# Kernel tuning notes

Measured on AMD Instinct MI355X. Metric: run time of the kernel, lower is better.

The kernel has to match this reference:

```python
import jax, jax.numpy as jnp
import numpy as np

H = 16        # num heads
DH = 128      # head dim
C = 64        # delta-rule chunk size
MAG = 0.5     # mag_weight
GATE_NORM = 16.0
EPS = 1e-6


def setup_inputs() -> dict:
    key = jax.random.key(0)
    ks = jax.random.split(key, 5)
    b, n, d = 2, 1024, H * DH
    s = d ** -0.5
    return {
        "x": jax.random.normal(ks[0], (b, n, d), jnp.float32),
        "Wq": jax.random.normal(ks[1], (d, d), jnp.float32) * s,
        "Wk": jax.random.normal(ks[2], (d, d), jnp.float32) * s,
        "Wv": jax.random.normal(ks[3], (d, d), jnp.float32) * s,
        "Wo": jax.random.normal(ks[4], (d, d), jnp.float32) * s,
    }


def _delta_rule_chunkwise(q, k, v, beta, chunk):
    # q,k,v: [b,h,l,d]; beta: [b,h,l,d] per-dim gate. Chunked DeltaNet parallel form.
    b, h, l, dk = q.shape
    dv = v.shape[-1]
    nc = l // chunk
    q = q * (dk ** -0.5)
    v = v * beta
    k_beta = k * beta
    qc, kc, vc, kbc = (a.reshape(b, h, nc, chunk, -1) for a in (q, k, v, k_beta))
    eye = jnp.eye(chunk, dtype=q.dtype)
    strict = jnp.tril(jnp.ones((chunk, chunk), bool), -1)
    # T = (I + strict_lower(k_beta k^T))^{-1} via triangular solve
    L = jnp.where(strict, kbc @ jnp.swapaxes(kc, -1, -2), 0.0)  # [b,h,nc,C,C]
    T = jax.scipy.linalg.solve_triangular(eye + L, jnp.broadcast_to(eye, L.shape), lower=True)
    u = T @ vc    # [b,h,nc,C,dv]
    w = T @ kbc   # [b,h,nc,C,dk]
    incl = jnp.tril(jnp.ones((chunk, chunk), bool))

    def step(S, inp):
        q_i, k_i, u_i, w_i = inp  # [b,h,C,d]
        u_i = u_i - w_i @ S
        attn = jnp.where(incl, q_i @ jnp.swapaxes(k_i, -1, -2), 0.0)
        o_i = q_i @ S + attn @ u_i
        S = S + jnp.swapaxes(k_i, -1, -2) @ u_i
        return S, o_i

    xs = tuple(jnp.moveaxis(a, 2, 0) for a in (qc, kc, u, w))
    S0 = jnp.zeros((b, h, dk, dv), q.dtype)
    S, o = jax.lax.scan(step, S0, xs)
    o = jnp.moveaxis(o, 0, 2).reshape(b, h, l, dv)
    return o, S


def _heads(t, b, n):
    return t.reshape(b, n, H, DH).transpose(0, 2, 1, 3)


def _base_attn(x, Wq, Wk, Wv, Wo):
    # vanilla causal softmax attention using the shared projections
    b, n, d = x.shape
    q, k, v = _heads(x @ Wq, b, n), _heads(x @ Wk, b, n), _heads(x @ Wv, b, n)
    scores = jnp.einsum('bhqd,bhkd->bhqk', q, k) / np.sqrt(DH).astype(np.float32)
    causal = jnp.tril(jnp.ones((n, n), bool))
    a = jax.nn.softmax(jnp.where(causal, scores, -jnp.inf), axis=-1)
    o = jnp.einsum('bhqk,bhkd->bhqd', a, v)
    return o.transpose(0, 2, 1, 3).reshape(b, n, d) @ Wo


def reference(x, Wq, Wk, Wv, Wo):
    b, n, d = x.shape
    k_raw = x @ Wk
    q = _heads(x @ Wq, b, n)
    k = _heads(k_raw, b, n)
    v = _heads(x @ Wv, b, n)
    g = _heads(k_raw, b, n)  # pool_g is identity: output_size == head_dim*num_kv_heads
    q = jnp.clip(jax.nn.softmax(q, axis=-1), EPS, 1.0 - EPS)
    k = jnp.clip(jax.nn.softmax(k, axis=-1), EPS, 1.0 - EPS)
    g = jnp.clip(jax.nn.log_sigmoid(g) / GATE_NORM, -GATE_NORM, GATE_NORM)
    o_lin, _ = _delta_rule_chunkwise(q.astype(jnp.float32), k.astype(jnp.float32),
                                     v.astype(jnp.float32), g.astype(jnp.float32), C)
    o_lin = o_lin.transpose(0, 2, 1, 3).reshape(b, n, d) @ Wo
    o_base = _base_attn(x, Wq, Wk, Wv, Wo)
    return MAG * o_lin + (1.0 - MAG) * o_base
```

## Files before the change

kernel.cpp:

```cpp
#include <hip/hip_runtime.h>
#include <hip/hip_bf16.h>
#include <math.h>

#define D 2048
#define NROWS 2048
#define NQKV 6144
#define H 16
#define DH 128
#define CHK 64
#define NC 16
#define EPSC 1e-6f
#define RSQDH 0.08838834764831845f

typedef unsigned short ushort_t;
typedef __attribute__((ext_vector_type(4))) float f4_t;
typedef __attribute__((ext_vector_type(8))) short s8_t;
typedef __attribute__((ext_vector_type(8))) _Float16 h8_t;
typedef __attribute__((ext_vector_type(4))) _Float16 h4_t;
typedef __attribute__((ext_vector_type(4))) unsigned short us4_t;

#define MFMA16(a, b, c) __builtin_amdgcn_mfma_f32_16x16x32_bf16((a), (b), (c), 0, 0, 0)
#define MFMAH(a, b, c)  __builtin_amdgcn_mfma_f32_16x16x32_f16((a), (b), (c), 0, 0, 0)
#define GLOAD16(g, l) __builtin_amdgcn_global_load_lds((const __attribute__((address_space(1))) unsigned int*)(g), (__attribute__((address_space(3))) unsigned int*)(l), 16, 0, 0)

__device__ __forceinline__ ushort_t f2bf(float f) {
  union { float f; unsigned u; } v; v.f = f;
  unsigned r = (v.u + 0x7fffu + ((v.u >> 16) & 1u)) >> 16;
  return (ushort_t)r;
}
__device__ __forceinline__ float bf2f(ushort_t h) {
  union { unsigned u; float f; } v; v.u = ((unsigned)h) << 16;
  return v.f;
}

__global__ __launch_bounds__(256) void split_h(const float* __restrict__ in,
                                               _Float16* __restrict__ hi) {
  int i = (blockIdx.x * 256 + threadIdx.x) * 4;
  float4 v = *(const float4*)(in + i);
  float vv[4] = {v.x, v.y, v.z, v.w};
  h4_t h;
#pragma unroll
  for (int j = 0; j < 4; j++) h[j] = (_Float16)vv[j];
  *(h4_t*)(hi + i) = h;
}

__global__ __launch_bounds__(256) void wsplit4(const float* __restrict__ Wq,
                                               const float* __restrict__ Wk,
                                               const float* __restrict__ Wv,
                                               const float* __restrict__ Wo,
                                               _Float16* __restrict__ Tqkv,
                                               _Float16* __restrict__ To) {
  __shared__ float t[32][33];
  const int tid = threadIdx.x;
  const int k0 = blockIdx.y * 32, n0 = blockIdx.x * 32;
  const int z = blockIdx.z;
  const float* W = (z == 0) ? Wq : (z == 1) ? Wk : (z == 2) ? Wv : Wo;
  _Float16* T = (z < 3) ? (Tqkv + (size_t)z * D * D) : To;
  const int c = tid & 31, rr = tid >> 5;
#pragma unroll
  for (int p = 0; p < 4; p++) {
    int r = p * 8 + rr;
    t[r][c] = W[(size_t)(k0 + r) * D + n0 + c];
  }
  __syncthreads();
#pragma unroll
  for (int p = 0; p < 4; p++) {
    int r = p * 8 + rr;
    T[(size_t)(n0 + r) * D + k0 + c] = (_Float16)t[c][r];
  }
}

__global__ __launch_bounds__(256) void gemm1(const _Float16* __restrict__ Ah,
                                             const _Float16* __restrict__ Bt,
                                             float* __restrict__ C,
                                             int M, int N, int K) {
  __shared__ __align__(16) ushort_t A_s[2][4096];
  __shared__ __align__(16) ushort_t B_s[2][4096];
  const int tid = threadIdx.x, lane = tid & 63, wid = tid >> 6;
  const int nwg = gridDim.x;
  int bid = blockIdx.x;
  int swz = (bid & 7) * (nwg >> 3) + (bid >> 3);
  const int nbn = N >> 7;
  const int bm = swz / nbn, bn = swz % nbn;
  const int row0 = bm << 7, col0 = bn << 7;
  const int lm = lane & 15, lg = lane >> 4;
  const int wrow = (wid >> 1) * 64, wcol = (wid & 1) * 64;
  const int NT = K >> 5;

  f4_t acc[4][4];
#pragma unroll
  for (int m = 0; m < 4; m++)
#pragma unroll
    for (int n = 0; n < 4; n++) acc[m][n] = (f4_t){0.f, 0.f, 0.f, 0.f};

  auto stage = [&](int buf, int ks) {
    int k0 = ks << 5;
#pragma unroll
    for (int p = 0; p < 2; p++) {
      int c = p * 256 + wid * 64 + lane;
      int r = c >> 2, q = (c & 3) * 8;
      char* la = (char*)&A_s[buf][0] + p * 4096 + wid * 1024;
      GLOAD16(Ah + (size_t)(row0 + r) * K + k0 + q, la);
      char* lb = (char*)&B_s[buf][0] + p * 4096 + wid * 1024;
      GLOAD16(Bt + (size_t)(col0 + r) * K + k0 + q, lb);
    }
  };

  stage(0, 0);
  __syncthreads();
  for (int t = 0; t < NT; t++) {
    int cur = t & 1;
    if (t + 1 < NT) stage(cur ^ 1, t + 1);
    h8_t af[4], bfr[4];
#pragma unroll
    for (int m = 0; m < 4; m++)
      af[m] = *(const h8_t*)&A_s[cur][(wrow + m * 16 + lm) * 32 + lg * 8];
#pragma unroll
    for (int n = 0; n < 4; n++)
      bfr[n] = *(const h8_t*)&B_s[cur][(wcol + n * 16 + lm) * 32 + lg * 8];
#pragma unroll
    for (int m = 0; m < 4; m++)
#pragma unroll
      for (int n = 0; n < 4; n++)
        acc[m][n] = MFMAH(af[m], bfr[n], acc[m][n]);
    __syncthreads();
  }
#pragma unroll
  for (int m = 0; m < 4; m++)
#pragma unroll
    for (int n = 0; n < 4; n++)
#pragma unroll
      for (int r = 0; r < 4; r++)
        C[(size_t)(row0 + wrow + m * 16 + lg * 4 + r) * N + col0 + wcol + n * 16 + lm] = acc[m][n][r];
}

__global__ __launch_bounds__(256) void gemm1h(const _Float16* __restrict__ Ah,
                                              const _Float16* __restrict__ Bt,
                                              _Float16* __restrict__ C,
                                              int M, int N, int K) {
  __shared__ __align__(16) ushort_t A_s[2][4096];
  __shared__ __align__(16) ushort_t B_s[2][4096];
  const int tid = threadIdx.x, lane = tid & 63, wid = tid >> 6;
  const int nwg = gridDim.x;
  int bid = blockIdx.x;
  int swz = (bid & 7) * (nwg >> 3) + (bid >> 3);
  const int nbn = N >> 7;
  const int bm = swz / nbn, bn = swz % nbn;
  const int lm = lane & 15, lg = lane >> 4;
  const int row0 = bm << 7, col0 = bn << 7;
  const int wrow = (wid >> 1) * 64, wcol = (wid & 1) * 64;
  const int NT = K >> 5;

  f4_t acc[4][4];
#pragma unroll
  for (int m = 0; m < 4; m++)
#pragma unroll
    for (int n = 0; n < 4; n++) acc[m][n] = (f4_t){0.f, 0.f, 0.f, 0.f};

  auto stage = [&](int buf, int ks) {
    int k0 = ks << 5;
#pragma unroll
    for (int p = 0; p < 2; p++) {
      int c = p * 256 + wid * 64 + lane;
      int r = c >> 2, q = (c & 3) * 8;
      char* la = (char*)&A_s[buf][0] + p * 4096 + wid * 1024;
      GLOAD16(Ah + (size_t)(row0 + r) * K + k0 + q, la);
      char* lb = (char*)&B_s[buf][0] + p * 4096 + wid * 1024;
      GLOAD16(Bt + (size_t)(col0 + r) * K + k0 + q, lb);
    }
  };

  stage(0, 0);
  __syncthreads();
  for (int t = 0; t < NT; t++) {
    int cur = t & 1;
    if (t + 1 < NT) stage(cur ^ 1, t + 1);
    h8_t af[4], bfr[4];
#pragma unroll
    for (int m = 0; m < 4; m++)
      af[m] = *(const h8_t*)&A_s[cur][(wrow + m * 16 + lm) * 32 + lg * 8];
#pragma unroll
    for (int n = 0; n < 4; n++)
      bfr[n] = *(const h8_t*)&B_s[cur][(wcol + n * 16 + lm) * 32 + lg * 8];
#pragma unroll
    for (int m = 0; m < 4; m++)
#pragma unroll
      for (int n = 0; n < 4; n++)
        acc[m][n] = MFMAH(af[m], bfr[n], acc[m][n]);
    __syncthreads();
  }
#pragma unroll
  for (int m = 0; m < 4; m++)
#pragma unroll
    for (int n = 0; n < 4; n++)
#pragma unroll
      for (int r = 0; r < 4; r++)
        C[(size_t)(row0 + wrow + m * 16 + lg * 4 + r) * N + col0 + wcol + n * 16 + lm] = (_Float16)acc[m][n][r];
}

__device__ __forceinline__ float gate_fn(float z) {
  float t = -z;
  float sp = (t > 20.f) ? t : log1pf(expf(t));
  float g = -sp * (1.f / 16.f);
  return fminf(fmaxf(g, -16.f), 16.f);
}

__global__ __launch_bounds__(256) void act_kernel(const _Float16* __restrict__ qkv,
                                                  float* __restrict__ qs,
                                                  float* __restrict__ ksm,
                                                  float* __restrict__ kb,
                                                  float* __restrict__ vb,
                                                  ushort_t* __restrict__ qb16,
                                                  ushort_t* __restrict__ kb16) {
  int wave = blockIdx.x * 4 + (threadIdx.x >> 6);
  int lane = threadIdx.x & 63;
  int row = wave >> 4, h = wave & 15;
  size_t inb = (size_t)row * NQKV + h * 128;
  size_t base = (size_t)wave * 128;
  float q0 = (float)qkv[inb + lane],        q1 = (float)qkv[inb + 64 + lane];
  float k0 = (float)qkv[inb + 2048 + lane], k1 = (float)qkv[inb + 2048 + 64 + lane];
  float v0 = (float)qkv[inb + 4096 + lane], v1 = (float)qkv[inb + 4096 + 64 + lane];

  qb16[base + lane] = f2bf(q0 * RSQDH);
  qb16[base + 64 + lane] = f2bf(q1 * RSQDH);
  kb16[base + lane] = f2bf(k0);
  kb16[base + 64 + lane] = f2bf(k1);

  float m = fmaxf(q0, q1);
  for (int o = 1; o < 64; o <<= 1) m = fmaxf(m, __shfl_xor(m, o));
  float e0 = expf(q0 - m), e1 = expf(q1 - m);
  float s = e0 + e1;
  for (int o = 1; o < 64; o <<= 1) s += __shfl_xor(s, o);
  float inv = 1.f / s;
  float qs0 = fminf(fmaxf(e0 * inv, EPSC), 1.f - EPSC) * RSQDH;
  float qs1 = fminf(fmaxf(e1 * inv, EPSC), 1.f - EPSC) * RSQDH;

  float mk = fmaxf(k0, k1);
  for (int o = 1; o < 64; o <<= 1) mk = fmaxf(mk, __shfl_xor(mk, o));
  float f0 = expf(k0 - mk), f1 = expf(k1 - mk);
  float sk = f0 + f1;
  for (int o = 1; o < 64; o <<= 1) sk += __shfl_xor(sk, o);
  float invk = 1.f / sk;
  float ks0 = fminf(fmaxf(f0 * invk, EPSC), 1.f - EPSC);
  float ks1 = fminf(fmaxf(f1 * invk, EPSC), 1.f - EPSC);

  float g0 = gate_fn(k0), g1 = gate_fn(k1);

  qs[base + lane] = qs0;        qs[base + 64 + lane] = qs1;
  ksm[base + lane] = ks0;       ksm[base + 64 + lane] = ks1;
  kb[base + lane] = ks0 * g0;   kb[base + 64 + lane] = ks1 * g1;
  vb[base + lane] = v0 * g0;    vb[base + 64 + lane] = v1 * g1;
}

__global__ __launch_bounds__(256) void k_transpose(const float* __restrict__ ksm,
                                                   ushort_t* __restrict__ kTh,
                                                   ushort_t* __restrict__ kTl) {
  __shared__ float t[32][33];
  const int tid = threadIdx.x;
  const int n0 = blockIdx.x * 32;
  const int d0 = blockIdx.y * 32;
  const int bh = blockIdx.z;
  const int b = bh >> 4, h = bh & 15;
  const int c = tid & 31, rr = tid >> 5;
#pragma unroll
  for (int p = 0; p < 4; p++) {
    int r = p * 8 + rr;
    t[r][c] = ksm[(size_t)(b * 1024 + n0 + r) * D + h * 128 + d0 + c];
  }
  __syncthreads();
#pragma unroll
  for (int p = 0; p < 4; p++) {
    int r = p * 8 + rr;
    float v = t[c][r];
    ushort_t hb = f2bf(v);
    kTh[(size_t)(bh * 128 + d0 + r) * 1024 + n0 + c] = hb;
    kTl[(size_t)(bh * 128 + d0 + r) * 1024 + n0 + c] = f2bf(v - bf2f(hb));
  }
}

__global__ __launch_bounds__(256) void chunk_uw_kernel(const float* __restrict__ qs,
                                                       const float* __restrict__ ksm,
                                                       const float* __restrict__ kb,
                                                       const float* __restrict__ vb,
                                                       float* __restrict__ u,
                                                       float* __restrict__ w,
                                                       ushort_t* __restrict__ attn_h,
                                                       ushort_t* __restrict__ attn_l) {
  __shared__ __align__(16) ushort_t kh_s[8192];
  __shared__ __align__(16) ushort_t kl_s[8192];
  __shared__ __align__(16) ushort_t xh_s[8192];
  __shared__ __align__(16) ushort_t xl_s[8192];
  __shared__ float L_s[4096];
  const int tid = threadIdx.x, lane = tid & 63, wid = tid >> 6;
  const int lm = lane & 15, lg = lane >> 4;
  const int bh = blockIdx.x >> 4, ci = blockIdx.x & 15;
  const int rowbase = (bh >> 4) * 1024 + ci * 64;
  const int colbase = (bh & 15) * 128;
  const size_t gbase = (size_t)rowbase * D + colbase;
  const int wr = (wid >> 1) * 32, wc = (wid & 1) * 32;

  auto stageM = [&](const float* __restrict__ src, ushort_t* dh, ushort_t* dl) {
#pragma unroll
    for (int it = 0; it < 4; it++) {
      int idx = tid + it * 256;
      int r = idx >> 4, c8 = idx & 15;
      const float* g = src + gbase + (size_t)r * D + c8 * 8;
      float4 v0 = *(const float4*)g;
      float4 v1 = *(const float4*)(g + 4);
      float vv[8] = {v0.x, v0.y, v0.z, v0.w, v1.x, v1.y, v1.z, v1.w};
      s8_t hv, lv;
#pragma unroll
      for (int j = 0; j < 8; j++) {
        ushort_t hb = f2bf(vv[j]);
        hv[j] = (short)hb;
        lv[j] = (short)f2bf(vv[j] - bf2f(hb));
      }
      int byo = r * 256 + ((c8 * 16) ^ ((r & 7) << 4));
      *(s8_t*)((char*)dh + byo) = hv;
      *(s8_t*)((char*)dl + byo) = lv;
    }
  };

  auto mm3 = [&](const ushort_t* Ah, const ushort_t* Al,
                 const ushort_t* Bh, const ushort_t* Bl, f4_t acc[2][2]) {
#pragma unroll
    for (int m = 0; m < 2; m++)
#pragma unroll
      for (int n = 0; n < 2; n++) acc[m][n] = (f4_t){0.f, 0.f, 0.f, 0.f};
#pragma unroll
    for (int term = 0; term < 3; term++) {
      const ushort_t* A = (term == 2) ? Al : Ah;
      const ushort_t* Bsrc = (term == 1) ? Bl : Bh;
#pragma unroll
      for (int ks = 0; ks < 4; ks++) {
        s8_t af[2], bf_[2];
#pragma unroll
        for (int m = 0; m < 2; m++) {
          int row = wr + m * 16 + lm;
          int byo = row * 256 + ((ks * 64 + lg * 16) ^ ((row & 7) << 4));
          af[m] = *(const s8_t*)((const char*)A + byo);
        }
#pragma unroll
        for (int n = 0; n < 2; n++) {
          int row = wc + n * 16 + lm;
          int byo = row * 256 + ((ks * 64 + lg * 16) ^ ((row & 7) << 4));
          bf_[n] = *(const s8_t*)((const char*)Bsrc + byo);
        }
#pragma unroll
        for (int m = 0; m < 2; m++)
#pragma unroll
          for (int n = 0; n < 2; n++)
            acc[m][n] = MFMA16(af[m], bf_[n], acc[m][n]);
      }
    }
  };

  stageM(ksm, kh_s, kl_s);
  stageM(kb, xh_s, xl_s);
  __syncthreads();

  f4_t accL[2][2];
  mm3(xh_s, xl_s, kh_s, kl_s, accL);
#pragma unroll
  for (int m = 0; m < 2; m++)
#pragma unroll
    for (int n = 0; n < 2; n++)
#pragma unroll
      for (int r = 0; r < 4; r++) {
        int i = wr + m * 16 + lg * 4 + r;
        int j = wc + n * 16 + lm;
        L_s[i * 64 + j] = (j < i) ? accL[m][n][r] : 0.f;
      }
  __syncthreads();

  stageM(qs, xh_s, xl_s);
  __syncthreads();

  f4_t accA[2][2];
  mm3(xh_s, xl_s, kh_s, kl_s, accA);
  ushort_t* abh = attn_h + (size_t)blockIdx.x * 4096;
  ushort_t* abl = attn_l + (size_t)blockIdx.x * 4096;
#pragma unroll
  for (int m = 0; m < 2; m++)
#pragma unroll
    for (int n = 0; n < 2; n++)
#pragma unroll
      for (int r = 0; r < 4; r++) {
        int i = wr + m * 16 + lg * 4 + r;
        int j = wc + n * 16 + lm;
        float val = (j <= i) ? accA[m][n][r] : 0.f;
        ushort_t hb = f2bf(val);
        abh[i * 64 + j] = hb;
        abl[i * 64 + j] = f2bf(val - bf2f(hb));
      }

  float x[64];
  const int c = tid & 127;
  const float* rhs = (tid < 128) ? (vb + gbase + c) : (kb + gbase + c);
#pragma unroll
  for (int j = 0; j < 64; j++) x[j] = rhs[(size_t)j * D];
#pragma unroll
  for (int i = 0; i < 64; i++) {
    float xi = x[i];
#pragma unroll
    for (int r2 = i + 1; r2 < 64; r2++) x[r2] -= L_s[r2 * 64 + i] * xi;
  }
  float* dst = (tid < 128) ? u : w;
#pragma unroll
  for (int j = 0; j < 64; j++) dst[gbase + (size_t)j * D + c] = x[j];
}

__global__ __launch_bounds__(512, 2) void scan_kernel(const float* __restrict__ qs,
                                                      const float* __restrict__ u,
                                                      const float* __restrict__ w,
                                                      const ushort_t* __restrict__ kTh_g,
                                                      const ushort_t* __restrict__ kTl_g,
                                                      const ushort_t* __restrict__ ath_g,
                                                      const ushort_t* __restrict__ atl_g,
                                                      float* __restrict__ o_lin) {
  __shared__ __align__(16) ushort_t kT_h[2][8192];
  __shared__ __align__(16) ushort_t kT_l[2][8192];
  __shared__ __align__(16) ushort_t at_h[2][4096];
  __shared__ __align__(16) ushort_t at_l[2][4096];
  __shared__ __align__(16) ushort_t Sh_s[16 * 128];
  __shared__ __align__(16) ushort_t Sl_s[16 * 128];
  __shared__ __align__(16) ushort_t uh_s[16 * 80];
  __shared__ __align__(16) ushort_t ul_s[16 * 80];
  __shared__ __align__(16) float oT[16 * 68];
  const int tid = threadIdx.x;
  const int bh = blockIdx.x;
  const int b = bh >> 4, h = bh & 15;
  const int g = blockIdx.y;
  const int colbase = h * 128;
  const int vcol = h * 128 + g * 16;
  const int lane = tid & 63, wid = tid >> 6;
  const int lm = lane & 15, lg = lane >> 4;
  const int dsub = lane >> 3;
  const int i8x = (lane & 7) ^ dsub;

  for (int i = tid; i < 16 * 128; i += 512) { Sh_s[i] = 0; Sl_s[i] = 0; }

  f4_t acc3[2];
  acc3[0] = (f4_t){0.f, 0.f, 0.f, 0.f};
  acc3[1] = (f4_t){0.f, 0.f, 0.f, 0.f};

  const ushort_t* kThb = kTh_g + (size_t)bh * 128 * 1024;
  const ushort_t* kTlb = kTl_g + (size_t)bh * 128 * 1024;

  auto issue_stage = [&](int buf, int chunk) {
#pragma unroll
    for (int it = 0; it < 2; it++) {
      int seg = it * 8 + wid;
      int d = seg * 8 + dsub;
      size_t goff = (size_t)d * 1024 + chunk * 64 + i8x * 8;
      GLOAD16(kThb + goff, (char*)&kT_h[buf][0] + seg * 1024);
      GLOAD16(kTlb + goff, (char*)&kT_l[buf][0] + seg * 1024);
    }
    {
      int i = wid * 8 + dsub;
      size_t asrc = (size_t)(bh * 16 + chunk) * 4096 + i * 64 + i8x * 8;
      GLOAD16(ath_g + asrc, (char*)&at_h[buf][0] + wid * 1024);
      GLOAD16(atl_g + asrc, (char*)&at_l[buf][0] + wid * 1024);
    }
  };

  const bool isU = (wid < 4);
  const int m0 = (isU ? wid : (wid - 4)) * 16;
  const float* Asrc = isU ? w : qs;

  float4 pA[4][2];
  float pu[4];
  auto prefetchA = [&](int chunk) {
    const size_t gb = (size_t)(b * 1024 + chunk * 64) * D;
#pragma unroll
    for (int ks = 0; ks < 4; ks++) {
      const float* ap = Asrc + gb + (size_t)(m0 + lm) * D + colbase + ks * 32 + lg * 8;
      pA[ks][0] = *(const float4*)ap;
      pA[ks][1] = *(const float4*)(ap + 4);
    }
    if (isU) {
#pragma unroll
      for (int r = 0; r < 4; r++)
        pu[r] = u[gb + (size_t)(m0 + lg * 4 + r) * D + vcol + lm];
    }
  };

  issue_stage(0, 0);
  prefetchA(0);
  __syncthreads();

  for (int chunk = 0; chunk < 16; chunk++) {
    const int cur = chunk & 1;
    const size_t gbase = (size_t)(b * 1024 + chunk * 64) * D;
    if (chunk + 1 < 16) issue_stage(cur ^ 1, chunk + 1);
    {
      f4_t acc = (f4_t){0.f, 0.f, 0.f, 0.f};
#pragma unroll
      for (int ks = 0; ks < 4; ks++) {
        float av[8] = {pA[ks][0].x, pA[ks][0].y, pA[ks][0].z, pA[ks][0].w,
                       pA[ks][1].x, pA[ks][1].y, pA[ks][1].z, pA[ks][1].w};
        s8_t ah, al;
#pragma unroll
        for (int j = 0; j < 8; j++) {
          ushort_t hb = f2bf(av[j]);
          ah[j] = (short)hb;
          al[j] = (short)f2bf(av[j] - bf2f(hb));
        }
        int byo = (lm * 256 + ks * 64 + lg * 16) ^ ((lm & 7) << 4);
        s8_t sh = *(const s8_t*)((const char*)Sh_s + byo);
        s8_t sl = *(const s8_t*)((const char*)Sl_s + byo);
        acc = MFMA16(ah, sh, acc);
        acc = MFMA16(ah, sl, acc);
        acc = MFMA16(al, sh, acc);
      }
      if (isU) {
        float res[4];
#pragma unroll
        for (int r = 0; r < 4; r++) res[r] = pu[r] - acc[r];
        us4_t rh, rl;
#pragma unroll
        for (int r = 0; r < 4; r++) {
          ushort_t hb = f2bf(res[r]);
          rh[r] = hb;
          rl[r] = f2bf(res[r] - bf2f(hb));
        }
        *(us4_t*)&uh_s[lm * 80 + m0 + lg * 4] = rh;
        *(us4_t*)&ul_s[lm * 80 + m0 + lg * 4] = rl;
      } else {
        float4 res = {acc[0], acc[1], acc[2], acc[3]};
        *(float4*)&oT[lm * 68 + m0 + lg * 4] = res;
      }
    }
    __syncthreads();
    if (chunk + 1 < 16) prefetchA(chunk + 1);
    if (isU) {
      float4 o0 = *(const float4*)&oT[lm * 68 + m0 + lg * 4];
      f4_t acc2 = (f4_t){o0.x, o0.y, o0.z, o0.w};
#pragma unroll
      for (int ks = 0; ks < 2; ks++) {
        int arow = m0 + lm;
        int abyo = arow * 128 + ((ks * 64 + lg * 16) ^ ((arow & 7) << 4));
        s8_t afh = *(const s8_t*)((const char*)&at_h[cur][0] + abyo);
        s8_t afl = *(const s8_t*)((const char*)&at_l[cur][0] + abyo);
        s8_t ufh = *(const s8_t*)&uh_s[lm * 80 + ks * 32 + lg * 8];
        s8_t ufl = *(const s8_t*)&ul_s[lm * 80 + ks * 32 + lg * 8];
        acc2 = MFMA16(afh, ufh, acc2);
        acc2 = MFMA16(afh, ufl, acc2);
        acc2 = MFMA16(afl, ufh, acc2);
      }
#pragma unroll
      for (int r = 0; r < 4; r++)
        o_lin[gbase + (size_t)(m0 + lg * 4 + r) * D + vcol + lm] = acc2[r];
    } else {
      const int w3 = wid - 4;
      s8_t ufh0 = *(const s8_t*)&uh_s[lm * 80 + 0 * 32 + lg * 8];
      s8_t ufl0 = *(const s8_t*)&ul_s[lm * 80 + 0 * 32 + lg * 8];
      s8_t ufh1 = *(const s8_t*)&uh_s[lm * 80 + 1 * 32 + lg * 8];
      s8_t ufl1 = *(const s8_t*)&ul_s[lm * 80 + 1 * 32 + lg * 8];
#pragma unroll
      for (int t = 0; t < 2; t++) {
        const int krow = (w3 * 2 + t) * 16 + lm;
        int b0 = krow * 128 + ((0 * 64 + lg * 16) ^ ((krow & 7) << 4));
        int b1 = krow * 128 + ((1 * 64 + lg * 16) ^ ((krow & 7) << 4));
        s8_t kh0 = *(const s8_t*)((const char*)&kT_h[cur][0] + b0);
        s8_t kl0 = *(const s8_t*)((const char*)&kT_l[cur][0] + b0);
        s8_t kh1 = *(const s8_t*)((const char*)&kT_h[cur][0] + b1);
        s8_t kl1 = *(const s8_t*)((const char*)&kT_l[cur][0] + b1);
        acc3[t] = MFMA16(ufh0, kh0, acc3[t]);
        acc3[t] = MFMA16(ufh0, kl0, acc3[t]);
        acc3[t] = MFMA16(ufl0, kh0, acc3[t]);
        acc3[t] = MFMA16(ufh1, kh1, acc3[t]);
        acc3[t] = MFMA16(ufh1, kl1, acc3[t]);
        acc3[t] = MFMA16(ufl1, kh1, acc3[t]);
      }
#pragma unroll
      for (int t = 0; t < 2; t++)
#pragma unroll
        for (int r = 0; r < 4; r++) {
          int c = lg * 4 + r;
          int k = (w3 * 2 + t) * 16 + lm;
          float sval = acc3[t][r];
          ushort_t hb = f2bf(sval);
          int sbyo = (c * 256 + k * 2) ^ ((c & 7) << 4);
          *(ushort_t*)((char*)Sh_s + sbyo) = hb;
          *(ushort_t*)((char*)Sl_s + sbyo) = f2bf(sval - bf2f(hb));
        }
    }
    __syncthreads();
  }
}

__global__ __launch_bounds__(256) void v_transpose(const _Float16* __restrict__ qkv,
                                                   ushort_t* __restrict__ vt) {
  __shared__ float t[32][33];
  const int tid = threadIdx.x;
  const int n0 = blockIdx.x * 32;
  const int d0 = blockIdx.y * 32;
  const int bh = blockIdx.z;
  const int b = bh >> 4, h = bh & 15;
  const int c = tid & 31, rr = tid >> 5;
#pragma unroll
  for (int p = 0; p < 4; p++) {
    int r = p * 8 + rr;
    t[r][c] = (float)qkv[(size_t)(b * 1024 + n0 + r) * NQKV + 4096 + h * 128 + d0 + c];
  }
  __syncthreads();
#pragma unroll
  for (int p = 0; p < 4; p++) {
    int r = p * 8 + rr;
    vt[(size_t)(bh * 128 + d0 + r) * 1024 + n0 + c] = f2bf(t[c][r]);
  }
}

__global__ __launch_bounds__(256) void attn_mfma(const ushort_t* __restrict__ qb,
                                                 const ushort_t* __restrict__ kb,
                                                 const ushort_t* __restrict__ vt,
                                                 const float* __restrict__ o_lin,
                                                 _Float16* __restrict__ mixh) {
  __shared__ __align__(16) ushort_t K_s[8192];
  __shared__ __align__(16) ushort_t V_s[8192];
  __shared__ __align__(16) ushort_t P_s[4][1152];
  const int tid = threadIdx.x;
  const int lane = tid & 63, wid = tid >> 6;
  const int bh = blockIdx.x;
  const int b = bh >> 4, h = bh & 15;
  const int qt = blockIdx.y;
  const int lm = lane & 15, lg = lane >> 4;

  s8_t qf[4];
  const size_t qrowG = (size_t)(b * 1024 + qt * 64 + wid * 16 + lm);
#pragma unroll
  for (int kb4 = 0; kb4 < 4; kb4++)
    qf[kb4] = *(const s8_t*)(qb + qrowG * D + h * 128 + kb4 * 32 + lg * 8);

  f4_t o[8];
#pragma unroll
  for (int n = 0; n < 8; n++) o[n] = (f4_t){0.f, 0.f, 0.f, 0.f};
  float mrow[4] = {-INFINITY, -INFINITY, -INFINITY, -INFINITY};
  float lrow[4] = {0.f, 0.f, 0.f, 0.f};
  const int myq = qt * 64 + wid * 16 + lg * 4;

  for (int kt = 0; kt <= qt; kt++) {
    __syncthreads();
#pragma unroll
    for (int p = 0; p < 4; p++) {
      int c = tid + p * 256;
      int key = c >> 4, dc = c & 15;
      s8_t v = *(const s8_t*)(kb + (size_t)(b * 1024 + kt * 64 + key) * D + h * 128 + dc * 8);
      int byo = key * 256 + ((dc * 16) ^ ((key & 7) << 4));
      *(s8_t*)((char*)K_s + byo) = v;
    }
#pragma unroll
    for (int p = 0; p < 4; p++) {
      int c = tid + p * 256;
      int d = c >> 3, nc = c & 7;
      s8_t v = *(const s8_t*)(vt + (size_t)(bh * 128 + d) * 1024 + kt * 64 + nc * 8);
      int byo = d * 128 + ((nc * 16) ^ ((d & 7) << 4));
      *(s8_t*)((char*)V_s + byo) = v;
    }
    __syncthreads();

    f4_t s[4];
#pragma unroll
    for (int ks = 0; ks < 4; ks++) {
      f4_t a = (f4_t){0.f, 0.f, 0.f, 0.f};
      int key = ks * 16 + lm;
#pragma unroll
      for (int kb4 = 0; kb4 < 4; kb4++) {
        int byo = key * 256 + ((kb4 * 64 + lg * 16) ^ ((key & 7) << 4));
        s8_t kf = *(const s8_t*)((char*)K_s + byo);
        a = MFMA16(qf[kb4], kf, a);
      }
      s[ks] = a;
    }
    if (kt == qt) {
#pragma unroll
      for (int ks = 0; ks < 4; ks++) {
        int key = kt * 64 + ks * 16 + lm;
#pragma unroll
        for (int r = 0; r < 4; r++)
          if (key > myq + r) s[ks][r] = -INFINITY;
      }
    }
    float mloc[4];
#pragma unroll
    for (int r = 0; r < 4; r++) {
      mloc[r] = fmaxf(fmaxf(s[0][r], s[1][r]), fmaxf(s[2][r], s[3][r]));
      mloc[r] = fmaxf(mloc[r], __shfl_xor(mloc[r], 1));
      mloc[r] = fmaxf(mloc[r], __shfl_xor(mloc[r], 2));
      mloc[r] = fmaxf(mloc[r], __shfl_xor(mloc[r], 4));
      mloc[r] = fmaxf(mloc[r], __shfl_xor(mloc[r], 8));
    }
    float scale[4];
#pragma unroll
    for (int r = 0; r < 4; r++) {
      float mn = fmaxf(mrow[r], mloc[r]);
      scale[r] = __expf(mrow[r] - mn);
      mrow[r] = mn;
    }
    float lad[4] = {0.f, 0.f, 0.f, 0.f};
#pragma unroll
    for (int ks = 0; ks < 4; ks++)
#pragma unroll
      for (int r = 0; r < 4; r++) {
        float p = __expf(s[ks][r] - mrow[r]);
        lad[r] += p;
        P_s[wid][(lg * 4 + r) * 72 + ks * 16 + lm] = f2bf(p);
      }
#pragma unroll
    for (int r = 0; r < 4; r++) {
      lad[r] += __shfl_xor(lad[r], 1);
      lad[r] += __shfl_xor(lad[r], 2);
      lad[r] += __shfl_xor(lad[r], 4);
      lad[r] += __shfl_xor(lad[r], 8);
      lrow[r] = lrow[r] * scale[r] + lad[r];
    }
#pragma unroll
    for (int n = 0; n < 8; n++)
#pragma unroll
      for (int r = 0; r < 4; r++) o[n][r] *= scale[r];

    s8_t pf[2];
#pragma unroll
    for (int ksl = 0; ksl < 2; ksl++)
      pf[ksl] = *(const s8_t*)&P_s[wid][lm * 72 + ksl * 32 + lg * 8];
#pragma unroll
    for (int n = 0; n < 8; n++) {
      int d = n * 16 + lm;
#pragma unroll
      for (int ksl = 0; ksl < 2; ksl++) {
        int byo = d * 128 + ((ksl * 64 + lg * 16) ^ ((d & 7) << 4));
        s8_t vf = *(const s8_t*)((char*)V_s + byo);
        o[n] = MFMA16(pf[ksl], vf, o[n]);
      }
    }
  }

  float invl[4];
#pragma unroll
  for (int r = 0; r < 4; r++) invl[r] = 1.f / lrow[r];
#pragma unroll
  for (int n = 0; n < 8; n++)
#pragma unroll
    for (int r = 0; r < 4; r++) {
      size_t G = (size_t)(b * 1024 + qt * 64 + wid * 16 + lg * 4 + r);
      int dcol = h * 128 + n * 16 + lm;
      float mix = 0.5f * (o[n][r] * invl[r]) + 0.5f * o_lin[G * D + dcol];
      mixh[G * D + dcol] = (_Float16)mix;
    }
}

extern "C" void kernel_launch(void* const* d_in, const int* in_sizes, int n_in,
                              void* d_out, int out_size, void* d_ws, size_t ws_size,
                              hipStream_t stream) {
  const float* x  = (const float*)d_in[0];
  const float* Wq = (const float*)d_in[1];
  const float* Wk = (const float*)d_in[2];
  const float* Wv = (const float*)d_in[3];
  const float* Wo = (const float*)d_in[4];
  float* out = (float*)d_out;
  float* ws = (float*)d_ws;

  const size_t B = (size_t)NROWS * D;
  _Float16* qkv = (_Float16*)(ws + 0 * B);
  float* q_s  = ws + 3 * B;
  float* k_sm = ws + 4 * B;
  float* kbuf = ws + 5 * B;
  float* vbuf = ws + 6 * B;
  float* u    = ws + 7 * B;
  float* w    = ws + 8 * B;
  float* o_lin = kbuf;

  _Float16* x_hi = (_Float16*)u;
  _Float16* Wt   = (_Float16*)(ws + 9 * B);
  ushort_t* attn_h = (ushort_t*)(ws + 9 * B);
  ushort_t* attn_l = attn_h + (size_t)2097152;
  ushort_t* kTh_g  = (ushort_t*)(ws + 9 * B + 2097152);
  ushort_t* kTl_g  = (ushort_t*)(ws + 10 * B);
  _Float16* Wo_t   = (_Float16*)(ws + 10 * B + 2097152);
  ushort_t* qb16 = (ushort_t*)q_s;
  qb16 = (ushort_t*)(ws + 2 * B);
  ushort_t* kb16 = qb16 + B;
  ushort_t* vt16 = (ushort_t*)vbuf;
  _Float16* mixh = (_Float16*)qkv;

  split_h<<<4096, 256, 0, stream>>>(x, x_hi);
  wsplit4<<<dim3(64, 64, 4), 256, 0, stream>>>(Wq, Wk, Wv, Wo, Wt, Wo_t);
  gemm1h<<<16 * 48, 256, 0, stream>>>(x_hi, Wt, qkv, NROWS, NQKV, D);

  act_kernel<<<8192, 256, 0, stream>>>(qkv, q_s, k_sm, kbuf, vbuf, qb16, kb16);
  k_transpose<<<dim3(32, 4, 32), 256, 0, stream>>>(k_sm, kTh_g, kTl_g);
  chunk_uw_kernel<<<512, 256, 0, stream>>>(q_s, k_sm, kbuf, vbuf, u, w, attn_h, attn_l);
  scan_kernel<<<dim3(32, 8), 512, 0, stream>>>(q_s, u, w, kTh_g, kTl_g, attn_h, attn_l, o_lin);

  v_transpose<<<dim3(32, 4, 32), 256, 0, stream>>>(qkv, vt16);
  attn_mfma<<<dim3(32, 16), 256, 0, stream>>>(qb16, kb16, vt16, o_lin, mixh);

  gemm1<<<16 * 16, 256, 0, stream>>>(mixh, Wo_t, out, NROWS, D, D);
}
```

Before: 302.1 us.

## Replace QKV projection GEMM with 256x256 tiled 8-wave pipelined kernel

Swaps the 128x128-tile, 4-wave fp16 GEMM for the QKV projection with a 256x256-tile, 8-wave kernel using K=64 steps and XOR-swizzled LDS layout. It splits A and B staging across phases, interleaves MFMA groups with barriers and s_setprio, and waits on vmcnt explicitly. The aim is more data reuse per tile, fewer LDS bank conflicts and better overlap of loads with MFMA. The grid drops to 192 workgroups on a 256-CU device, which may underfill the GPU, and the larger LDS and register use lowers occupancy.

```diff
diff --git a/kernel.cpp b/kernel.cpp
--- a/kernel.cpp
+++ b/kernel.cpp
@@ -134,68 +134,169 @@
         C[(size_t)(row0 + wrow + m * 16 + lg * 4 + r) * N + col0 + wcol + n * 16 + lm] = acc[m][n][r];
 }
 
-__global__ __launch_bounds__(256) void gemm1h(const _Float16* __restrict__ Ah,
-                                              const _Float16* __restrict__ Bt,
-                                              _Float16* __restrict__ C,
-                                              int M, int N, int K) {
-  __shared__ __align__(16) ushort_t A_s[2][4096];
-  __shared__ __align__(16) ushort_t B_s[2][4096];
+__global__ __launch_bounds__(512, 2) void gemm8(const _Float16* __restrict__ Ah,
+                                                const _Float16* __restrict__ Bt,
+                                                _Float16* __restrict__ C,
+                                                int M, int N, int K) {
+  __shared__ __align__(16) ushort_t A_s[2][16384];
+  __shared__ __align__(16) ushort_t B_s[2][16384];
   const int tid = threadIdx.x, lane = tid & 63, wid = tid >> 6;
   const int nwg = gridDim.x;
   int bid = blockIdx.x;
   int swz = (bid & 7) * (nwg >> 3) + (bid >> 3);
-  const int nbn = N >> 7;
+  const int nbn = N >> 8;
   const int bm = swz / nbn, bn = swz % nbn;
+  const int row0 = bm << 8, col0 = bn << 8;
   const int lm = lane & 15, lg = lane >> 4;
-  const int row0 = bm << 7, col0 = bn << 7;
-  const int wrow = (wid >> 1) * 64, wcol = (wid & 1) * 64;
-  const int NT = K >> 5;
-
-  f4_t acc[4][4];
-#pragma unroll
-  for (int m = 0; m < 4; m++)
+  const int wr = wid >> 2, wc = wid & 3;
+  const int NT = K >> 6;
+
+  f4_t acc[8][4];
+#pragma unroll
+  for (int m = 0; m < 8; m++)
 #pragma unroll
     for (int n = 0; n < 4; n++) acc[m][n] = (f4_t){0.f, 0.f, 0.f, 0.f};
 
-  auto stage = [&](int buf, int ks) {
-    int k0 = ks << 5;
-#pragma unroll
-    for (int p = 0; p < 2; p++) {
-      int c = p * 256 + wid * 64 + lane;
-      int r = c >> 2, q = (c & 3) * 8;
-      char* la = (char*)&A_s[buf][0] + p * 4096 + wid * 1024;
-      GLOAD16(Ah + (size_t)(row0 + r) * K + k0 + q, la);
-      char* lb = (char*)&B_s[buf][0] + p * 4096 + wid * 1024;
-      GLOAD16(Bt + (size_t)(col0 + r) * K + k0 + q, lb);
+  auto stageA = [&](int buf, int t) {
+    int k0 = t << 6;
+#pragma unroll
+    for (int p = 0; p < 4; p++) {
+      int c = p * 512 + tid;
+      int r = c >> 3, q = c & 7;
+      int qx = q ^ (r & 7);
+      GLOAD16(Ah + (size_t)(row0 + r) * K + k0 + qx * 8, (char*)&A_s[buf][0] + c * 16);
     }
   };
-
-  stage(0, 0);
-  __syncthreads();
+  auto stageB = [&](int buf, int t) {
+    int k0 = t << 6;
+#pragma unroll
+    for (int p = 0; p < 4; p++) {
+      int c = p * 512 + tid;
+      int r = c >> 3, q = c & 7;
+      int qx = q ^ (r & 7);
+      GLOAD16(Bt + (size_t)(col0 + r) * K + k0 + qx * 8, (char*)&B_s[buf][0] + c * 16);
+    }
+  };
+
+  stageA(0, 0);
+  stageB(0, 0);
+  asm volatile("s_waitcnt vmcnt(0)" ::: "memory");
+  __builtin_amdgcn_s_barrier();
+  __builtin_amdgcn_sched_barrier(0);
+
   for (int t = 0; t < NT; t++) {
-    int cur = t & 1;
-    if (t + 1 < NT) stage(cur ^ 1, t + 1);
-    h8_t af[4], bfr[4];
-#pragma unroll
-    for (int m = 0; m < 4; m++)
-      af[m] = *(const h8_t*)&A_s[cur][(wrow + m * 16 + lm) * 32 + lg * 8];
+    const int cur = t & 1;
+    const char* As = (const char*)&A_s[cur][0];
+    const char* Bs = (const char*)&B_s[cur][0];
+    h8_t bfr[4][2];
+    if (t + 1 < NT) {
+      stageA(cur ^ 1, t + 1);
+      asm volatile("s_waitcnt vmcnt(4)" ::: "memory");
+    } else {
+      asm volatile("s_waitcnt vmcnt(0)" ::: "memory");
+    }
+    __builtin_amdgcn_s_barrier();
+    __builtin_amdgcn_sched_barrier(0);
 #pragma unroll
     for (int n = 0; n < 4; n++)
-      bfr[n] = *(const h8_t*)&B_s[cur][(wcol + n * 16 + lm) * 32 + lg * 8];
-#pragma unroll
-    for (int m = 0; m < 4; m++)
-#pragma unroll
-      for (int n = 0; n < 4; n++)
-        acc[m][n] = MFMAH(af[m], bfr[n], acc[m][n]);
-    __syncthreads();
-  }
-#pragma unroll
-  for (int m = 0; m < 4; m++)
+#pragma unroll
+      for (int ks = 0; ks < 2; ks++) {
+        int row = wc * 64 + n * 16 + lm;
+        bfr[n][ks] = *(const h8_t*)(Bs + row * 128 + (((ks * 4 + lg) ^ (row & 7)) << 4));
+      }
+    {
+      h8_t af[2][2];
+#pragma unroll
+      for (int mm = 0; mm < 2; mm++)
+#pragma unroll
+        for (int ks = 0; ks < 2; ks++) {
+          int row = wr * 128 + (0 + mm) * 16 + lm;
+          af[mm][ks] = *(const h8_t*)(As + row * 128 + (((ks * 4 + lg) ^ (row & 7)) << 4));
+        }
+      __builtin_amdgcn_s_setprio(1);
+#pragma unroll
+      for (int mm = 0; mm < 2; mm++)
+#pragma unroll
+        for (int n = 0; n < 4; n++)
+#pragma unroll
+          for (int ks = 0; ks < 2; ks++)
+            acc[0 + mm][n] = MFMAH(af[mm][ks], bfr[n][ks], acc[0 + mm][n]);
+      __builtin_amdgcn_s_setprio(0);
+    }
+    __builtin_amdgcn_s_barrier();
+    __builtin_amdgcn_sched_barrier(0);
+    if (t + 1 < NT) stageB(cur ^ 1, t + 1);
+    {
+      h8_t af[2][2];
+#pragma unroll
+      for (int mm = 0; mm < 2; mm++)
+#pragma unroll
+        for (int ks = 0; ks < 2; ks++) {
+          int row = wr * 128 + (2 + mm) * 16 + lm;
+          af[mm][ks] = *(const h8_t*)(As + row * 128 + (((ks * 4 + lg) ^ (row & 7)) << 4));
+        }
+      __builtin_amdgcn_s_setprio(1);
+#pragma unroll
+      for (int mm = 0; mm < 2; mm++)
+#pragma unroll
+        for (int n = 0; n < 4; n++)
+#pragma unroll
+          for (int ks = 0; ks < 2; ks++)
+            acc[2 + mm][n] = MFMAH(af[mm][ks], bfr[n][ks], acc[2 + mm][n]);
+      __builtin_amdgcn_s_setprio(0);
+    }
+    __builtin_amdgcn_s_barrier();
+    __builtin_amdgcn_sched_barrier(0);
+    {
+      h8_t af[2][2];
+#pragma unroll
+      for (int mm = 0; mm < 2; mm++)
+#pragma unroll
+        for (int ks = 0; ks < 2; ks++) {
+          int row = wr * 128 + (4 + mm) * 16 + lm;
+          af[mm][ks] = *(const h8_t*)(As + row * 128 + (((ks * 4 + lg) ^ (row & 7)) << 4));
+        }
+      __builtin_amdgcn_s_setprio(1);
+#pragma unroll
+      for (int mm = 0; mm < 2; mm++)
+#pragma unroll
+        for (int n = 0; n < 4; n++)
+#pragma unroll
+          for (int ks = 0; ks < 2; ks++)
+            acc[4 + mm][n] = MFMAH(af[mm][ks], bfr[n][ks], acc[4 + mm][n]);
+      __builtin_amdgcn_s_setprio(0);
+    }
+    __builtin_amdgcn_s_barrier();
+    __builtin_amdgcn_sched_barrier(0);
+    {
+      h8_t af[2][2];
+#pragma unroll
+      for (int mm = 0; mm < 2; mm++)
+#pragma unroll
+        for (int ks = 0; ks < 2; ks++) {
+          int row = wr * 128 + (6 + mm) * 16 + lm;
+          af[mm][ks] = *(const h8_t*)(As + row * 128 + (((ks * 4 + lg) ^ (row & 7)) << 4));
+        }
+      __builtin_amdgcn_s_setprio(1);
+#pragma unroll
+      for (int mm = 0; mm < 2; mm++)
+#pragma unroll
+        for (int n = 0; n < 4; n++)
+#pragma unroll
+          for (int ks = 0; ks < 2; ks++)
+            acc[6 + mm][n] = MFMAH(af[mm][ks], bfr[n][ks], acc[6 + mm][n]);
+      __builtin_amdgcn_s_setprio(0);
+    }
+    __builtin_amdgcn_s_barrier();
+    __builtin_amdgcn_sched_barrier(0);
+  }
+#pragma unroll
+  for (int m = 0; m < 8; m++)
 #pragma unroll
     for (int n = 0; n < 4; n++)
 #pragma unroll
       for (int r = 0; r < 4; r++)
-        C[(size_t)(row0 + wrow + m * 16 + lg * 4 + r) * N + col0 + wcol + n * 16 + lm] = (_Float16)acc[m][n][r];
+        C[(size_t)(row0 + wr * 128 + m * 16 + lg * 4 + r) * N + col0 + wc * 64 + n * 16 + lm] = (_Float16)acc[m][n][r];
 }
 
 __device__ __forceinline__ float gate_fn(float z) {
@@ -778,15 +879,14 @@
   ushort_t* kTh_g  = (ushort_t*)(ws + 9 * B + 2097152);
   ushort_t* kTl_g  = (ushort_t*)(ws + 10 * B);
   _Float16* Wo_t   = (_Float16*)(ws + 10 * B + 2097152);
-  ushort_t* qb16 = (ushort_t*)q_s;
-  qb16 = (ushort_t*)(ws + 2 * B);
+  ushort_t* qb16 = (ushort_t*)(ws + 2 * B);
   ushort_t* kb16 = qb16 + B;
   ushort_t* vt16 = (ushort_t*)vbuf;
   _Float16* mixh = (_Float16*)qkv;
 
   split_h<<<4096, 256, 0, stream>>>(x, x_hi);
   wsplit4<<<dim3(64, 64, 4), 256, 0, stream>>>(Wq, Wk, Wv, Wo, Wt, Wo_t);
-  gemm1h<<<16 * 48, 256, 0, stream>>>(x_hi, Wt, qkv, NROWS, NQKV, D);
+  gemm8<<<8 * 24, 512, 0, stream>>>(x_hi, Wt, qkv, NROWS, NQKV, D);
 
   act_kernel<<<8192, 256, 0, stream>>>(qkv, q_s, k_sm, kbuf, vbuf, qb16, kb16);
   k_transpose<<<dim3(32, 4, 32), 256, 0, stream>>>(k_sm, kTh_g, kTl_g);
```

Result: slower. 322.9 us (+6.9%).
